# Kernel optimization log

Measured on AMD Instinct MI355X. Metric: run time of the kernel, lower is better.

## Reference

```python
import jax, jax.numpy as jnp
import numpy as np

N = 40000      # total nodes in the batched graph
E = 640000     # total edges (avg degree 16)
F_IN = 1280    # num_features (ESM embedding dim)
H = 128        # hidden_dim
G = 64         # number of graphs in the batch
OUT = 273      # output_dim (GO terms)
NEG_SLOPE = 0.2
BN_EPS = 1e-5


def setup_inputs() -> dict:
    key = jax.random.key(0)
    ks = jax.random.split(key, 16)
    def nrm(k, shape, s=0.05):
        return jax.random.normal(k, shape, dtype=jnp.float32) * s
    inp = {}
    inp["x"] = jax.random.normal(ks[0], (N, F_IN), dtype=jnp.float32)
    inp["edge_index"] = jax.random.randint(ks[1], (2, E), 0, N, dtype=jnp.int32)
    inp["batch"] = jnp.sort(jax.random.randint(ks[2], (N,), 0, G, dtype=jnp.int32))
    inp["W1"] = nrm(ks[3], (F_IN, H)); inp["b1"] = jnp.zeros((H,), jnp.float32)
    inp["a_src1"] = nrm(ks[4], (H,)); inp["a_dst1"] = nrm(ks[5], (H,))
    inp["W2"] = nrm(ks[6], (H, H)); inp["b2"] = jnp.zeros((H,), jnp.float32)
    inp["a_src2"] = nrm(ks[7], (H,)); inp["a_dst2"] = nrm(ks[8], (H,))
    inp["W3"] = nrm(ks[9], (H, H)); inp["b3"] = jnp.zeros((H,), jnp.float32)
    inp["a_src3"] = nrm(ks[10], (H,)); inp["a_dst3"] = nrm(ks[11], (H,))
    inp["fc1_W"] = nrm(ks[12], (H, 1024)); inp["fc1_b"] = jnp.zeros((1024,), jnp.float32)
    inp["bn_g"] = jnp.ones((1024,), jnp.float32); inp["bn_b"] = jnp.zeros((1024,), jnp.float32)
    inp["bn_rm"] = jnp.zeros((1024,), jnp.float32); inp["bn_rv"] = jnp.ones((1024,), jnp.float32)
    inp["fc2_W"] = nrm(ks[13], (1024, OUT)); inp["fc2_b"] = jnp.zeros((OUT,), jnp.float32)
    return inp


def gat_layer(x, W, b, a_src, a_dst, src, dst, n_nodes):
    # single-head GAT ('gat_originated'): h = xW, e_ij = lrelu(a_src.h_j + a_dst.h_i)
    h = x @ W                                            # [N, H]
    e = jax.nn.leaky_relu((h @ a_src)[src] + (h @ a_dst)[dst], NEG_SLOPE)  # [E]
    # numerically-stable segment softmax over incoming edges of each target node
    m = jax.ops.segment_max(e, dst, num_segments=n_nodes)
    p = jnp.exp(e - m[dst])
    denom = jax.ops.segment_sum(p, dst, num_segments=n_nodes)
    alpha = p / (denom[dst] + 1e-16)                     # [E]
    out = jax.ops.segment_sum(alpha[:, None] * h[src], dst, num_segments=n_nodes)
    return out + b


def reference(x, edge_index, batch, W1, b1, a_src1, a_dst1, W2, b2, a_src2, a_dst2,
              W3, b3, a_src3, a_dst3, fc1_W, fc1_b, bn_g, bn_b, bn_rm, bn_rv, fc2_W, fc2_b):
    n = x.shape[0]
    src, dst = edge_index[0], edge_index[1]
    h = jax.nn.relu(gat_layer(x, W1, b1, a_src1, a_dst1, src, dst, n))
    h = jax.nn.relu(gat_layer(h, W2, b2, a_src2, a_dst2, src, dst, n))
    h = gat_layer(h, W3, b3, a_src3, a_dst3, src, dst, n)
    # gap: global mean pool per graph
    cnt = jax.ops.segment_sum(jnp.ones((n,), h.dtype), batch, num_segments=G)
    pooled = jax.ops.segment_sum(h, batch, num_segments=G) / jnp.maximum(cnt, 1.0)[:, None]
    z = pooled @ fc1_W + fc1_b                            # [G, 1024]
    z = (z - bn_rm) * jax.lax.rsqrt(bn_rv + BN_EPS) * bn_g + bn_b  # BN eval mode
    z = jax.nn.relu(z)                                    # dropout is identity in eval
    return jax.nn.sigmoid(z @ fc2_W + fc2_b)              # [G, 273]
```

## Files before the change

### kernel.cpp

```cpp
#include <hip/hip_runtime.h>
#include <math.h>

#define N_NODES 40000
#define N_EDGES 640000
#define F_IN    1280
#define H       128
#define NG      64
#define OUTD    273
#define FC1D    1024
#define NEG_SLOPE 0.2f
#define BN_EPS  1e-5f

typedef __attribute__((ext_vector_type(8))) short short8;
typedef __attribute__((ext_vector_type(4))) float f32x4;

__device__ __forceinline__ unsigned short f2bf(float f) {
    unsigned u = __float_as_uint(f);
    u += 0x7FFF + ((u >> 16) & 1);
    return (unsigned short)(u >> 16);
}
__device__ __forceinline__ float bf2f(unsigned short s) {
    return __uint_as_float((unsigned)s << 16);
}

__global__ void edge_hist(const int* __restrict__ dst, int* __restrict__ cnt, int e) {
    int i = blockIdx.x * blockDim.x + threadIdx.x;
    if (i < e) atomicAdd(&cnt[dst[i]], 1);
}

__global__ void scan_excl(const int* __restrict__ cnt, int* __restrict__ row_ptr, int n) {
    const int CH = 40;
    __shared__ int sm[1024];
    int tid = threadIdx.x;
    int start = tid * CH;
    int local[CH];
    int s = 0;
    #pragma unroll
    for (int k = 0; k < CH; ++k) {
        int i = start + k;
        int v = (i < n) ? cnt[i] : 0;
        local[k] = s;
        s += v;
    }
    sm[tid] = s;
    __syncthreads();
    for (int off = 1; off < 1024; off <<= 1) {
        int t = (tid >= off) ? sm[tid - off] : 0;
        __syncthreads();
        sm[tid] += t;
        __syncthreads();
    }
    int base = sm[tid] - s;
    #pragma unroll
    for (int k = 0; k < CH; ++k) {
        int i = start + k;
        if (i < n) row_ptr[i] = base + local[k];
    }
    if (tid == 1023) row_ptr[n] = sm[1023];
}

__global__ void edge_fill(const int* __restrict__ src, const int* __restrict__ dst,
                          const int* __restrict__ row_ptr, int* __restrict__ fill,
                          int* __restrict__ csr_src, int e) {
    int i = blockIdx.x * blockDim.x + threadIdx.x;
    if (i < e) {
        int d = dst[i];
        int pos = row_ptr[d] + atomicAdd(&fill[d], 1);
        csr_src[pos] = src[i];
    }
}

__device__ __forceinline__ void wprep_one(const float* __restrict__ W,
                                          unsigned short* __restrict__ Bp,
                                          int i, int K) {
    int k = i >> 7, col = i & 127;
    float v = W[i];
    unsigned short hh = f2bf(v);
    unsigned short ll = f2bf(v - bf2f(hh));
    int t = k >> 6, rr = k & 63;
    int s = rr >> 5, r5 = rr & 31;
    int laneHi = r5 >> 3, j = r5 & 7;
    int lane = laneHi * 16 + (col & 15);
    int n = col >> 4;
    int U = (n * 2 + s) * 64 + lane;
    size_t idx = (size_t)t * 16384 + (size_t)U * 8 + j;
    Bp[idx] = hh;
    Bp[idx + 8192] = ll;
}

__global__ void wprep_all(const float* __restrict__ W1, const float* __restrict__ W2,
                          const float* __restrict__ W3, unsigned short* __restrict__ Bp1,
                          unsigned short* __restrict__ Bp2, unsigned short* __restrict__ Bp3) {
    int i = blockIdx.x * blockDim.x + threadIdx.x;
    const int n1 = F_IN * H, n2 = H * H;
    if (i < n1) { wprep_one(W1, Bp1, i, F_IN); return; }
    i -= n1;
    if (i < n2) { wprep_one(W2, Bp2, i, H); return; }
    i -= n2;
    if (i < n2) { wprep_one(W3, Bp3, i, H); }
}

__device__ __forceinline__ void cvt8(float4 x, float4 y, short8& hi, short8& lo) {
    float f[8] = {x.x, x.y, x.z, x.w, y.x, y.y, y.z, y.w};
    #pragma unroll
    for (int j = 0; j < 8; ++j) {
        unsigned u = __float_as_uint(f[j]);
        unsigned short hh = (unsigned short)((u + 0x7FFF + ((u >> 16) & 1)) >> 16);
        hi[j] = (short)hh;
        float r = f[j] - __uint_as_float((unsigned)hh << 16);
        unsigned ur = __float_as_uint(r);
        lo[j] = (short)((ur + 0x7FFF + ((ur >> 16) & 1)) >> 16);
    }
}

__global__ __launch_bounds__(256) void gemm_fused(
    const float* __restrict__ A, const unsigned short* __restrict__ Bp,
    const float* __restrict__ a_src, const float* __restrict__ a_dst,
    unsigned short* __restrict__ hWb, float* __restrict__ hs,
    float* __restrict__ hd, int K)
{
    __shared__ __align__(16) unsigned short lds[2][16384];
    const int tid  = threadIdx.x;
    const int lane = tid & 63, wv = tid >> 6;
    const int fr = lane & 15, q = lane >> 4;
    const int m0 = blockIdx.x * 64;
    const int row = m0 + wv * 16 + fr;
    const int nt = K >> 6;

    const uint4* gb = (const uint4*)Bp + tid;
    const float* Aptr = A + (size_t)row * K + q * 8;

    f32x4 acc0 = {}, acc1 = {}, acc2 = {}, acc3 = {},
          acc4 = {}, acc5 = {}, acc6 = {}, acc7 = {};

    uint4 bA0, bA1, bA2, bA3, bA4, bA5, bA6, bA7;
    uint4 bB0, bB1, bB2, bB3, bB4, bB5, bB6, bB7;
    float4 aA0, aA1, aA2, aA3, aB0, aB1, aB2, aB3;

#define LOADB(t, r0, r1, r2, r3, r4, r5, r6, r7)                                \
    { const uint4* g = gb + (size_t)(t) * 2048;                                 \
      r0 = g[0];    r1 = g[256];  r2 = g[512];  r3 = g[768];                    \
      r4 = g[1024]; r5 = g[1280]; r6 = g[1536]; r7 = g[1792]; }
#define LOADA(t, x0, x1, x2, x3)                                                \
    { const float* ap = Aptr + (size_t)(t) * 64;                                \
      x0 = *(const float4*)(ap);      x1 = *(const float4*)(ap + 4);            \
      x2 = *(const float4*)(ap + 32); x3 = *(const float4*)(ap + 36); }
#define STAGE(buf, r0, r1, r2, r3, r4, r5, r6, r7)                              \
    { uint4* lp = (uint4*)lds[buf] + tid;                                       \
      lp[0] = r0;    lp[256] = r1;  lp[512] = r2;  lp[768] = r3;                \
      lp[1024] = r4; lp[1280] = r5; lp[1536] = r6; lp[1792] = r7; }
#define MSTEP(buf, nn, accv, ss)                                                \
    { const short8 bh = *(const short8*)&lds[buf][(size_t)(((nn)*2+(ss))*64 + lane)*8];        \
      const short8 bl = *(const short8*)&lds[buf][(size_t)(((nn)*2+(ss))*64 + lane)*8 + 8192]; \
      accv = __builtin_amdgcn_mfma_f32_16x16x32_bf16(ah, bh, accv, 0, 0, 0);    \
      accv = __builtin_amdgcn_mfma_f32_16x16x32_bf16(ah, bl, accv, 0, 0, 0);    \
      accv = __builtin_amdgcn_mfma_f32_16x16x32_bf16(al, bh, accv, 0, 0, 0); }
#define COMPUTE(buf, x0, x1, x2, x3)                                            \
    { short8 ah, al;                                                            \
      cvt8(x0, x1, ah, al);                                                     \
      MSTEP(buf, 0, acc0, 0) MSTEP(buf, 1, acc1, 0) MSTEP(buf, 2, acc2, 0)      \
      MSTEP(buf, 3, acc3, 0) MSTEP(buf, 4, acc4, 0) MSTEP(buf, 5, acc5, 0)      \
      MSTEP(buf, 6, acc6, 0) MSTEP(buf, 7, acc7, 0)                             \
      cvt8(x2, x3, ah, al);                                                     \
      MSTEP(buf, 0, acc0, 1) MSTEP(buf, 1, acc1, 1) MSTEP(buf, 2, acc2, 1)      \
      MSTEP(buf, 3, acc3, 1) MSTEP(buf, 4, acc4, 1) MSTEP(buf, 5, acc5, 1)      \
      MSTEP(buf, 6, acc6, 1) MSTEP(buf, 7, acc7, 1) }

    LOADB(0, bA0, bA1, bA2, bA3, bA4, bA5, bA6, bA7);
    LOADA(0, aA0, aA1, aA2, aA3);

    for (int t = 0; t < nt; t += 2) {
        STAGE(0, bA0, bA1, bA2, bA3, bA4, bA5, bA6, bA7);
        LOADB(t + 1, bB0, bB1, bB2, bB3, bB4, bB5, bB6, bB7);
        LOADA(t + 1, aB0, aB1, aB2, aB3);
        __syncthreads();
        COMPUTE(0, aA0, aA1, aA2, aA3);

        STAGE(1, bB0, bB1, bB2, bB3, bB4, bB5, bB6, bB7);
        if (t + 2 < nt) {
            LOADB(t + 2, bA0, bA1, bA2, bA3, bA4, bA5, bA6, bA7);
            LOADA(t + 2, aA0, aA1, aA2, aA3);
        }
        __syncthreads();
        COMPUTE(1, aB0, aB1, aB2, aB3);
    }
#undef LOADB
#undef LOADA
#undef STAGE
#undef MSTEP
#undef COMPUTE

    const int rb = m0 + wv * 16 + q * 4;
#define EPI(nn, accv)                                                           \
    {                                                                           \
        _Pragma("unroll")                                                       \
        for (int i = 0; i < 4; ++i)                                             \
            hWb[(size_t)(rb + i) * H + (nn)*16 + fr] = f2bf(accv[i]);           \
    }
    EPI(0, acc0) EPI(1, acc1) EPI(2, acc2) EPI(3, acc3)
    EPI(4, acc4) EPI(5, acc5) EPI(6, acc6) EPI(7, acc7)
#undef EPI

    float asv[8], adv[8];
    #pragma unroll
    for (int n = 0; n < 8; ++n) {
        asv[n] = a_src[n * 16 + fr];
        adv[n] = a_dst[n * 16 + fr];
    }
    #pragma unroll
    for (int i = 0; i < 4; ++i) {
        float ss = acc0[i]*asv[0] + acc1[i]*asv[1] + acc2[i]*asv[2] + acc3[i]*asv[3]
                 + acc4[i]*asv[4] + acc5[i]*asv[5] + acc6[i]*asv[6] + acc7[i]*asv[7];
        float dd = acc0[i]*adv[0] + acc1[i]*adv[1] + acc2[i]*adv[2] + acc3[i]*adv[3]
                 + acc4[i]*adv[4] + acc5[i]*adv[5] + acc6[i]*adv[6] + acc7[i]*adv[7];
        #pragma unroll
        for (int off = 8; off; off >>= 1) {
            ss += __shfl_xor(ss, off);
            dd += __shfl_xor(dd, off);
        }
        if (fr == 0) { hs[rb + i] = ss; hd[rb + i] = dd; }
    }
}

__device__ __forceinline__ float bfhi(unsigned u) { return __uint_as_float(u << 16); }
__device__ __forceinline__ float bflo(unsigned u) { return __uint_as_float(u & 0xffff0000u); }

__global__ void attn_agg(const unsigned short* __restrict__ hWb,
                         const float* __restrict__ hs, const float* __restrict__ hd,
                         const int* __restrict__ row_ptr, const int* __restrict__ csr_src,
                         const float* __restrict__ bias, float* __restrict__ out,
                         int n, int relu_flag) {
    int wv = (blockIdx.x * blockDim.x + threadIdx.x) >> 6;
    int lane = threadIdx.x & 63;
    if (wv >= n) return;
    int p0 = row_ptr[wv], p1 = row_ptr[wv + 1];
    int deg = p1 - p0;
    float hdi = hd[wv];
    float ax = 0.f, ay = 0.f;
    const unsigned* hb = (const unsigned*)hWb;

    if (deg <= 64) {
        int valid = (lane < deg);
        int sidx = valid ? csr_src[p0 + lane] : 0;

#define PF(k) int s_##k = __shfl(sidx, k); unsigned u_##k = 0;                  \
              if (deg > k) u_##k = hb[(size_t)s_##k * 64 + lane];
        PF(0)  PF(1)  PF(2)  PF(3)  PF(4)  PF(5)  PF(6)  PF(7)
        PF(8)  PF(9)  PF(10) PF(11) PF(12) PF(13) PF(14) PF(15)
#undef PF

        float e = hs[sidx] + hdi;
        e = (e >= 0.f) ? e : NEG_SLOPE * e;
        float m = valid ? e : -3.4e38f;
        #pragma unroll
        for (int off = 32; off; off >>= 1) m = fmaxf(m, __shfl_xor(m, off));
        float pe = valid ? __expf(e - m) : 0.f;
        float dsum = pe;
        #pragma unroll
        for (int off = 32; off; off >>= 1) dsum += __shfl_xor(dsum, off);
        pe *= 1.f / (dsum + 1e-16f);

#define AC(k) if (deg > k) { float aa = __shfl(pe, k);                          \
                             ax += aa * bfhi(u_##k); ay += aa * bflo(u_##k); }
        AC(0)  AC(1)  AC(2)  AC(3)  AC(4)  AC(5)  AC(6)  AC(7)
        AC(8)  AC(9)  AC(10) AC(11) AC(12) AC(13) AC(14) AC(15)
#undef AC

        for (int j = 16; j < deg; j += 4) {
            int t0 = __shfl(sidx, j);
            int t1 = (j + 1 < deg) ? __shfl(sidx, j + 1) : t0;
            int t2 = (j + 2 < deg) ? __shfl(sidx, j + 2) : t0;
            int t3 = (j + 3 < deg) ? __shfl(sidx, j + 3) : t0;
            unsigned v0 = hb[(size_t)t0 * 64 + lane];
            unsigned v1 = hb[(size_t)t1 * 64 + lane];
            unsigned v2 = hb[(size_t)t2 * 64 + lane];
            unsigned v3 = hb[(size_t)t3 * 64 + lane];
            float b0 = __shfl(pe, j);
            float b1 = (j + 1 < deg) ? __shfl(pe, j + 1) : 0.f;
            float b2 = (j + 2 < deg) ? __shfl(pe, j + 2) : 0.f;
            float b3 = (j + 3 < deg) ? __shfl(pe, j + 3) : 0.f;
            ax += b0 * bfhi(v0); ay += b0 * bflo(v0);
            ax += b1 * bfhi(v1); ay += b1 * bflo(v1);
            ax += b2 * bfhi(v2); ay += b2 * bflo(v2);
            ax += b3 * bfhi(v3); ay += b3 * bflo(v3);
        }
    } else {
        float m = -3.4e38f;
        for (int p = p0 + lane; p < p1; p += 64) {
            float e = hs[csr_src[p]] + hdi;
            e = (e >= 0.f) ? e : NEG_SLOPE * e;
            m = fmaxf(m, e);
        }
        #pragma unroll
        for (int off = 32; off; off >>= 1) m = fmaxf(m, __shfl_xor(m, off));
        float dsum = 0.f;
        for (int p = p0 + lane; p < p1; p += 64) {
            float e = hs[csr_src[p]] + hdi;
            e = (e >= 0.f) ? e : NEG_SLOPE * e;
            dsum += __expf(e - m);
        }
        #pragma unroll
        for (int off = 32; off; off >>= 1) dsum += __shfl_xor(dsum, off);
        float inv = 1.f / (dsum + 1e-16f);
        for (int p = p0; p < p1; ++p) {
            int s = csr_src[p];
            float e = hs[s] + hdi;
            e = (e >= 0.f) ? e : NEG_SLOPE * e;
            float alpha = __expf(e - m) * inv;
            unsigned u = hb[(size_t)s * 64 + lane];
            ax += alpha * bfhi(u); ay += alpha * bflo(u);
        }
    }
    float2 bv = *(const float2*)&bias[2 * lane];
    float o0 = ax + bv.x;
    float o1 = ay + bv.y;
    if (relu_flag) { o0 = fmaxf(o0, 0.f); o1 = fmaxf(o1, 0.f); }
    float2 ov; ov.x = o0; ov.y = o1;
    *(float2*)&out[(size_t)wv * H + 2 * lane] = ov;
}

__device__ __forceinline__ void graph_range(const int* __restrict__ batch, int n,
                                            int g, int& start, int& end) {
    int lo = 0, hi = n;
    while (lo < hi) { int mid = (lo + hi) >> 1; if (batch[mid] < g) lo = mid + 1; else hi = mid; }
    start = lo;
    lo = start; hi = n;
    while (lo < hi) { int mid = (lo + hi) >> 1; if (batch[mid] < g + 1) lo = mid + 1; else hi = mid; }
    end = lo;
}

__global__ void pool_part(const float* __restrict__ h, const int* __restrict__ batch,
                          float* __restrict__ part, int n) {
    int g = blockIdx.x >> 3, c = blockIdx.x & 7;
    int f = threadIdx.x;
    int start, end;
    graph_range(batch, n, g, start, end);
    int len = end - start;
    int cs = start + (len * c) / 8, ce = start + (len * (c + 1)) / 8;
    float acc = 0.f;
    for (int i = cs; i < ce; ++i) acc += h[(size_t)i * H + f];
    part[((size_t)g * 8 + c) * H + f] = acc;
}

__global__ void pool_final(const float* __restrict__ part, const int* __restrict__ batch,
                           float* __restrict__ pooled, int n) {
    int g = blockIdx.x;
    int f = threadIdx.x;
    int start, end;
    graph_range(batch, n, g, start, end);
    float s = 0.f;
    #pragma unroll
    for (int c = 0; c < 8; ++c) s += part[((size_t)g * 8 + c) * H + f];
    float cnt = (float)(end - start);
    pooled[g * H + f] = s / fmaxf(cnt, 1.f);
}

__global__ void fc1_bn_relu(const float* __restrict__ pooled, const float* __restrict__ W,
                            const float* __restrict__ b, const float* __restrict__ bng,
                            const float* __restrict__ bnb, const float* __restrict__ bnrm,
                            const float* __restrict__ bnrv, float* __restrict__ z) {
    int g = blockIdx.x >> 2;
    int j = ((blockIdx.x & 3) << 8) + threadIdx.x;
    const float* pr = pooled + g * H;
    float acc = b[j];
    #pragma unroll 8
    for (int k = 0; k < H; ++k) acc += pr[k] * W[k * FC1D + j];
    float v = (acc - bnrm[j]) * rsqrtf(bnrv[j] + BN_EPS) * bng[j] + bnb[j];
    z[g * FC1D + j] = fmaxf(v, 0.f);
}

__global__ void fc2_sig(const float* __restrict__ z, const float* __restrict__ W,
                        const float* __restrict__ b, float* __restrict__ out) {
    int g = blockIdx.x;
    int j = threadIdx.x;
    if (j >= OUTD) return;
    const float* zr = z + g * FC1D;
    float acc = b[j];
    #pragma unroll 4
    for (int k = 0; k < FC1D; ++k) acc += zr[k] * W[k * OUTD + j];
    out[g * OUTD + j] = 1.f / (1.f + __expf(-acc));
}

extern "C" void kernel_launch(void* const* d_in, const int* in_sizes, int n_in,
                              void* d_out, int out_size, void* d_ws, size_t ws_size,
                              hipStream_t stream) {
    const float* x     = (const float*)d_in[0];
    const int*   eidx  = (const int*)d_in[1];
    const int*   batch = (const int*)d_in[2];
    const float* W1 = (const float*)d_in[3];  const float* b1 = (const float*)d_in[4];
    const float* as1 = (const float*)d_in[5]; const float* ad1 = (const float*)d_in[6];
    const float* W2 = (const float*)d_in[7];  const float* b2 = (const float*)d_in[8];
    const float* as2 = (const float*)d_in[9]; const float* ad2 = (const float*)d_in[10];
    const float* W3 = (const float*)d_in[11]; const float* b3 = (const float*)d_in[12];
    const float* as3 = (const float*)d_in[13]; const float* ad3 = (const float*)d_in[14];
    const float* fc1W = (const float*)d_in[15]; const float* fc1b = (const float*)d_in[16];
    const float* bng = (const float*)d_in[17];  const float* bnb = (const float*)d_in[18];
    const float* bnrm = (const float*)d_in[19]; const float* bnrv = (const float*)d_in[20];
    const float* fc2W = (const float*)d_in[21]; const float* fc2b = (const float*)d_in[22];
    const int* src = eidx;
    const int* dst = eidx + N_EDGES;

    float* hA      = (float*)d_ws;
    float* hs      = hA + (size_t)N_NODES * H;
    float* hd      = hs + N_NODES;
    float* pooled  = hd + N_NODES;
    float* part    = pooled + NG * H;
    float* z       = part + NG * 8 * H;
    unsigned short* hWb = (unsigned short*)(z + NG * FC1D);
    unsigned short* Bp1 = hWb + (size_t)N_NODES * H;
    unsigned short* Bp2 = Bp1 + (size_t)(F_IN / 64) * 16384;
    unsigned short* Bp3 = Bp2 + (size_t)(H / 64) * 16384;
    int*   row_ptr = (int*)(Bp3 + (size_t)(H / 64) * 16384);
    int*   row_cnt = row_ptr + (N_NODES + 1);
    int*   csr_src = row_cnt + N_NODES;

    const int EB = (N_EDGES + 255) / 256;
    const int NW = (N_NODES * 64 + 255) / 256;
    const int GB = N_NODES / 64;

    const int WTOT = F_IN * H + 2 * H * H;
    wprep_all<<<(WTOT + 255) / 256, 256, 0, stream>>>(W1, W2, W3, Bp1, Bp2, Bp3);

    hipMemsetAsync(row_cnt, 0, N_NODES * sizeof(int), stream);
    edge_hist<<<EB, 256, 0, stream>>>(dst, row_cnt, N_EDGES);
    scan_excl<<<1, 1024, 0, stream>>>(row_cnt, row_ptr, N_NODES);
    hipMemsetAsync(row_cnt, 0, N_NODES * sizeof(int), stream);
    edge_fill<<<EB, 256, 0, stream>>>(src, dst, row_ptr, row_cnt, csr_src, N_EDGES);

    gemm_fused<<<GB, 256, 0, stream>>>(x, Bp1, as1, ad1, hWb, hs, hd, F_IN);
    attn_agg<<<NW, 256, 0, stream>>>(hWb, hs, hd, row_ptr, csr_src, b1, hA, N_NODES, 1);
    gemm_fused<<<GB, 256, 0, stream>>>(hA, Bp2, as2, ad2, hWb, hs, hd, H);
    attn_agg<<<NW, 256, 0, stream>>>(hWb, hs, hd, row_ptr, csr_src, b2, hA, N_NODES, 1);
    gemm_fused<<<GB, 256, 0, stream>>>(hA, Bp3, as3, ad3, hWb, hs, hd, H);
    attn_agg<<<NW, 256, 0, stream>>>(hWb, hs, hd, row_ptr, csr_src, b3, hA, N_NODES, 0);

    pool_part<<<NG * 8, H, 0, stream>>>(hA, batch, part, N_NODES);
    pool_final<<<NG, H, 0, stream>>>(part, batch, pooled, N_NODES);
    fc1_bn_relu<<<NG * 4, 256, 0, stream>>>(pooled, fc1W, fc1b, bng, bnb, bnrm, bnrv, z);
    fc2_sig<<<NG, 320, 0, stream>>>(z, fc2W, fc2b, (float*)d_out);
}
```

Before: 742.8 us.

## Single-buffer GEMM LDS, hoist hs load, fuse pool_final into fc1

The GEMM's LDS tile goes from double to single buffering, halving shared memory per block (possibly raising occupancy) but adding two extra barriers per iteration. In attention aggregation the hs[sidx] load is issued before the neighbour prefetch so its latency overlaps. The pool_final kernel is folded into fc1_bn_relu, which now reduces the partial sums into shared memory itself, removing one launch and the pooled buffer at the cost of recomputing the reduction in each of the four blocks per graph.

```diff
diff --git a/kernel.cpp b/kernel.cpp
--- a/kernel.cpp
+++ b/kernel.cpp
@@ -119,7 +119,7 @@
     unsigned short* __restrict__ hWb, float* __restrict__ hs,
     float* __restrict__ hd, int K)
 {
-    __shared__ __align__(16) unsigned short lds[2][16384];
+    __shared__ __align__(16) unsigned short lds[16384];
     const int tid  = threadIdx.x;
     const int lane = tid & 63, wv = tid >> 6;
     const int fr = lane & 15, q = lane >> 4;
@@ -145,44 +145,45 @@
     { const float* ap = Aptr + (size_t)(t) * 64;                                \
       x0 = *(const float4*)(ap);      x1 = *(const float4*)(ap + 4);            \
       x2 = *(const float4*)(ap + 32); x3 = *(const float4*)(ap + 36); }
-#define STAGE(buf, r0, r1, r2, r3, r4, r5, r6, r7)                              \
-    { uint4* lp = (uint4*)lds[buf] + tid;                                       \
+#define STAGE(r0, r1, r2, r3, r4, r5, r6, r7)                                   \
+    { uint4* lp = (uint4*)lds + tid;                                            \
       lp[0] = r0;    lp[256] = r1;  lp[512] = r2;  lp[768] = r3;                \
       lp[1024] = r4; lp[1280] = r5; lp[1536] = r6; lp[1792] = r7; }
-#define MSTEP(buf, nn, accv, ss)                                                \
-    { const short8 bh = *(const short8*)&lds[buf][(size_t)(((nn)*2+(ss))*64 + lane)*8];        \
-      const short8 bl = *(const short8*)&lds[buf][(size_t)(((nn)*2+(ss))*64 + lane)*8 + 8192]; \
+#define MSTEP(nn, accv, ss)                                                     \
+    { const short8 bh = *(const short8*)&lds[(size_t)(((nn)*2+(ss))*64 + lane)*8];        \
+      const short8 bl = *(const short8*)&lds[(size_t)(((nn)*2+(ss))*64 + lane)*8 + 8192]; \
       accv = __builtin_amdgcn_mfma_f32_16x16x32_bf16(ah, bh, accv, 0, 0, 0);    \
       accv = __builtin_amdgcn_mfma_f32_16x16x32_bf16(ah, bl, accv, 0, 0, 0);    \
       accv = __builtin_amdgcn_mfma_f32_16x16x32_bf16(al, bh, accv, 0, 0, 0); }
-#define COMPUTE(buf, x0, x1, x2, x3)                                            \
+#define COMPUTE(x0, x1, x2, x3)                                                 \
     { short8 ah, al;                                                            \
       cvt8(x0, x1, ah, al);                                                     \
-      MSTEP(buf, 0, acc0, 0) MSTEP(buf, 1, acc1, 0) MSTEP(buf, 2, acc2, 0)      \
-      MSTEP(buf, 3, acc3, 0) MSTEP(buf, 4, acc4, 0) MSTEP(buf, 5, acc5, 0)      \
-      MSTEP(buf, 6, acc6, 0) MSTEP(buf, 7, acc7, 0)                             \
+      MSTEP(0, acc0, 0) MSTEP(1, acc1, 0) MSTEP(2, acc2, 0)                     \
+      MSTEP(3, acc3, 0) MSTEP(4, acc4, 0) MSTEP(5, acc5, 0)                     \
+      MSTEP(6, acc6, 0) MSTEP(7, acc7, 0)                                       \
       cvt8(x2, x3, ah, al);                                                     \
-      MSTEP(buf, 0, acc0, 1) MSTEP(buf, 1, acc1, 1) MSTEP(buf, 2, acc2, 1)      \
-      MSTEP(buf, 3, acc3, 1) MSTEP(buf, 4, acc4, 1) MSTEP(buf, 5, acc5, 1)      \
-      MSTEP(buf, 6, acc6, 1) MSTEP(buf, 7, acc7, 1) }
+      MSTEP(0, acc0, 1) MSTEP(1, acc1, 1) MSTEP(2, acc2, 1)                     \
+      MSTEP(3, acc3, 1) MSTEP(4, acc4, 1) MSTEP(5, acc5, 1)                     \
+      MSTEP(6, acc6, 1) MSTEP(7, acc7, 1) }
 
     LOADB(0, bA0, bA1, bA2, bA3, bA4, bA5, bA6, bA7);
     LOADA(0, aA0, aA1, aA2, aA3);
 
     for (int t = 0; t < nt; t += 2) {
-        STAGE(0, bA0, bA1, bA2, bA3, bA4, bA5, bA6, bA7);
+        STAGE(bA0, bA1, bA2, bA3, bA4, bA5, bA6, bA7);
         LOADB(t + 1, bB0, bB1, bB2, bB3, bB4, bB5, bB6, bB7);
         LOADA(t + 1, aB0, aB1, aB2, aB3);
         __syncthreads();
-        COMPUTE(0, aA0, aA1, aA2, aA3);
-
-        STAGE(1, bB0, bB1, bB2, bB3, bB4, bB5, bB6, bB7);
+        COMPUTE(aA0, aA1, aA2, aA3);
+        __syncthreads();
+        STAGE(bB0, bB1, bB2, bB3, bB4, bB5, bB6, bB7);
         if (t + 2 < nt) {
             LOADB(t + 2, bA0, bA1, bA2, bA3, bA4, bA5, bA6, bA7);
             LOADA(t + 2, aA0, aA1, aA2, aA3);
         }
         __syncthreads();
-        COMPUTE(1, aB0, aB1, aB2, aB3);
+        COMPUTE(aB0, aB1, aB2, aB3);
+        __syncthreads();
     }
 #undef LOADB
 #undef LOADA
@@ -242,6 +243,7 @@
     if (deg <= 64) {
         int valid = (lane < deg);
         int sidx = valid ? csr_src[p0 + lane] : 0;
+        float hsv = hs[sidx];
 
 #define PF(k) int s_##k = __shfl(sidx, k); unsigned u_##k = 0;                  \
               if (deg > k) u_##k = hb[(size_t)s_##k * 64 + lane];
@@ -249,7 +251,7 @@
         PF(8)  PF(9)  PF(10) PF(11) PF(12) PF(13) PF(14) PF(15)
 #undef PF
 
-        float e = hs[sidx] + hdi;
+        float e = hsv + hdi;
         e = (e >= 0.f) ? e : NEG_SLOPE * e;
         float m = valid ? e : -3.4e38f;
         #pragma unroll
@@ -342,26 +344,24 @@
     part[((size_t)g * 8 + c) * H + f] = acc;
 }
 
-__global__ void pool_final(const float* __restrict__ part, const int* __restrict__ batch,
-                           float* __restrict__ pooled, int n) {
-    int g = blockIdx.x;
-    int f = threadIdx.x;
-    int start, end;
-    graph_range(batch, n, g, start, end);
-    float s = 0.f;
-    #pragma unroll
-    for (int c = 0; c < 8; ++c) s += part[((size_t)g * 8 + c) * H + f];
-    float cnt = (float)(end - start);
-    pooled[g * H + f] = s / fmaxf(cnt, 1.f);
-}
-
-__global__ void fc1_bn_relu(const float* __restrict__ pooled, const float* __restrict__ W,
-                            const float* __restrict__ b, const float* __restrict__ bng,
-                            const float* __restrict__ bnb, const float* __restrict__ bnrm,
-                            const float* __restrict__ bnrv, float* __restrict__ z) {
+__global__ void fc1_bn_relu(const float* __restrict__ part, const int* __restrict__ batch,
+                            const float* __restrict__ W, const float* __restrict__ b,
+                            const float* __restrict__ bng, const float* __restrict__ bnb,
+                            const float* __restrict__ bnrm, const float* __restrict__ bnrv,
+                            float* __restrict__ z, int n) {
+    __shared__ float pr[H];
     int g = blockIdx.x >> 2;
-    int j = ((blockIdx.x & 3) << 8) + threadIdx.x;
-    const float* pr = pooled + g * H;
+    int tid = threadIdx.x;
+    if (tid < H) {
+        int start, end;
+        graph_range(batch, n, g, start, end);
+        float s = 0.f;
+        #pragma unroll
+        for (int c = 0; c < 8; ++c) s += part[((size_t)g * 8 + c) * H + tid];
+        pr[tid] = s / fmaxf((float)(end - start), 1.f);
+    }
+    __syncthreads();
+    int j = ((blockIdx.x & 3) << 8) + tid;
     float acc = b[j];
     #pragma unroll 8
     for (int k = 0; k < H; ++k) acc += pr[k] * W[k * FC1D + j];
@@ -403,8 +403,7 @@
     float* hA      = (float*)d_ws;
     float* hs      = hA + (size_t)N_NODES * H;
     float* hd      = hs + N_NODES;
-    float* pooled  = hd + N_NODES;
-    float* part    = pooled + NG * H;
+    float* part    = hd + N_NODES;
     float* z       = part + NG * 8 * H;
     unsigned short* hWb = (unsigned short*)(z + NG * FC1D);
     unsigned short* Bp1 = hWb + (size_t)N_NODES * H;
@@ -435,7 +434,6 @@
     attn_agg<<<NW, 256, 0, stream>>>(hWb, hs, hd, row_ptr, csr_src, b3, hA, N_NODES, 0);
 
     pool_part<<<NG * 8, H, 0, stream>>>(hA, batch, part, N_NODES);
-    pool_final<<<NG, H, 0, stream>>>(part, batch, pooled, N_NODES);
-    fc1_bn_relu<<<NG * 4, 256, 0, stream>>>(pooled, fc1W, fc1b, bng, bnb, bnrm, bnrv, z);
+    fc1_bn_relu<<<NG * 4, 256, 0, stream>>>(part, batch, fc1W, fc1b, bng, bnb, bnrm, bnrv, z, N_NODES);
     fc2_sig<<<NG, 320, 0, stream>>>(z, fc2W, fc2b, (float*)d_out);
 }
```

After: 739.0 us. About the same (-0.5%).
